# Kernel optimization log

Hardware: AMD Instinct MI355X
Metric: run time of the kernel (lower is better)

Reference implementation:

```python
import jax, jax.numpy as jnp
import numpy as np

B, S, D_IN, D_K, D_V = 4, 2048, 1024, 1024, 1024


def setup_inputs() -> dict:
    key = jax.random.key(0)
    ks = jax.random.split(key, 7)
    s_in = 1.0 / np.sqrt(D_IN)
    return {
        "x": jax.random.normal(ks[0], (B, S, D_IN), dtype=jnp.float32),
        "Wq": jax.random.uniform(ks[1], (D_K, D_IN), jnp.float32, -s_in, s_in),
        "bq": jax.random.uniform(ks[2], (D_K,), jnp.float32, -s_in, s_in),
        "Wk": jax.random.uniform(ks[3], (D_K, D_IN), jnp.float32, -s_in, s_in),
        "bk": jax.random.uniform(ks[4], (D_K,), jnp.float32, -s_in, s_in),
        "Wv": jax.random.uniform(ks[5], (D_V, D_IN), jnp.float32, -s_in, s_in),
        "bv": jax.random.uniform(ks[6], (D_V,), jnp.float32, -s_in, s_in),
    }


def reference(x, Wq, bq, Wk, bk, Wv, bv):
    # Linear: y = x @ W^T + b (torch convention, weight is [out, in])
    Q = jnp.einsum("bsd,kd->bsk", x, Wq) + bq  # [B,S,Dk]
    K = jnp.einsum("bsd,kd->bsk", x, Wk) + bk  # [B,S,Dk]
    V = jnp.einsum("bsd,vd->bsv", x, Wv) + bv  # [B,S,Dv]
    norm_fact = 1.0 / np.sqrt(D_K)
    # NOTE: faithful to original — softmax on raw scores, THEN scale by 1/sqrt(dim_k)
    scores = jnp.einsum("bqk,bsk->bqs", Q, K)          # [B,S,S]
    atten = jax.nn.softmax(scores, axis=-1) * norm_fact  # post-softmax scaling
    return jnp.einsum("bqs,bsv->bqv", atten, V)          # [B,S,Dv]
```

## Files before the change

### kernel.cpp

```cpp
#include <hip/hip_runtime.h>
#include <hip/hip_bf16.h>
#include <cstdint>
#include <cstddef>


typedef __attribute__((ext_vector_type(8))) _Float16 f16x8;
typedef __attribute__((ext_vector_type(4))) _Float16 f16x4;
typedef __attribute__((ext_vector_type(4))) float f32x4;

#define BM 128
#define BN 128
#define BK 64

#define NBATCH 4
#define SEQ 2048
#define DIM 1024
#define MTOT (NBATCH * SEQ)

__device__ __forceinline__ void async_ld16(const void* g, void* l) {
  __builtin_amdgcn_global_load_lds((__attribute__((address_space(1))) void*)(g),
                                   (__attribute__((address_space(3))) void*)(l),
                                   16, 0, 0);
}

__device__ __forceinline__ void gemm_core(const _Float16* __restrict__ A, int lda,
                                          const _Float16* __restrict__ B, int ldb,
                                          int K, int m0, int n0,
                                          _Float16* As, _Float16* Bs,
                                          f32x4 (&acc)[4][4]) {
  const int t = threadIdx.x;
  const int w = t >> 6;
  const int lrow = t & 15;
  const int quad = (t >> 4) & 3;
  const int wm = (w >> 1) << 6;
  const int wn = (w & 1) << 6;

  const int rb = t >> 3;
  const int co = (((t & 7) ^ (rb & 7)) << 3);
  const _Float16* Ap = A + (size_t)(m0 + rb) * lda + co;
  const _Float16* Bp = B + (size_t)(n0 + rb) * ldb + co;

  const int sw = lrow & 7;

  for (int k0 = 0; k0 < K; k0 += BK) {
#pragma unroll
    for (int i = 0; i < 4; ++i)
      async_ld16(Ap + (size_t)(i * 32) * lda + k0, As + i * 2048 + (w << 9));
#pragma unroll
    for (int i = 0; i < 4; ++i)
      async_ld16(Bp + (size_t)(i * 32) * ldb + k0, Bs + i * 2048 + (w << 9));
    __syncthreads();
#pragma unroll
    for (int kk = 0; kk < BK; kk += 32) {
      const int slot = ((kk >> 3) + quad) ^ sw;
      f16x8 af[4], bfr[4];
#pragma unroll
      for (int mi = 0; mi < 4; ++mi)
        af[mi] = *(const f16x8*)(As + (wm + mi * 16 + lrow) * BK + (slot << 3));
#pragma unroll
      for (int ni = 0; ni < 4; ++ni)
        bfr[ni] = *(const f16x8*)(Bs + (wn + ni * 16 + lrow) * BK + (slot << 3));
#pragma unroll
      for (int mi = 0; mi < 4; ++mi)
#pragma unroll
        for (int ni = 0; ni < 4; ++ni)
          acc[mi][ni] = __builtin_amdgcn_mfma_f32_16x16x32_f16(af[mi], bfr[ni],
                                                              acc[mi][ni], 0, 0, 0);
    }
    __syncthreads();
  }
}

__global__ __launch_bounds__(256) void split_all_kernel(
    const float* __restrict__ x, const float* __restrict__ Wq,
    const float* __restrict__ Wk, const float* __restrict__ Wv,
    _Float16* __restrict__ xh, _Float16* __restrict__ Wqh,
    _Float16* __restrict__ Wkh, _Float16* __restrict__ Wvh) {
  int r = blockIdx.x;
  const float* src;
  _Float16* dst;
  if (r < MTOT)            { src = x;  dst = xh;  }
  else if (r < MTOT + DIM) { src = Wq; dst = Wqh; r -= MTOT; }
  else if (r < MTOT + 2 * DIM) { src = Wk; dst = Wkh; r -= MTOT + DIM; }
  else                     { src = Wv; dst = Wvh; r -= MTOT + 2 * DIM; }
  const int t = threadIdx.x;
  const float4 v = ((const float4*)(src + (size_t)r * DIM))[t];
  f16x4 hi = {(_Float16)v.x, (_Float16)v.y, (_Float16)v.z, (_Float16)v.w};
  ((f16x4*)(dst + (size_t)r * DIM))[t] = hi;
}

__global__ __launch_bounds__(256, 2) void qkv_kernel(
    const _Float16* __restrict__ xh,
    const _Float16* __restrict__ Wqh, const float* __restrict__ bq,
    const _Float16* __restrict__ Wkh, const float* __restrict__ bk,
    const _Float16* __restrict__ Wvh, const float* __restrict__ bv,
    _Float16* __restrict__ Qp, _Float16* __restrict__ Kp,
    _Float16* __restrict__ Vt) {
  __shared__ alignas(16) _Float16 As[BM * BK];
  __shared__ alignas(16) _Float16 Bs[BN * BK];
  f32x4 acc[4][4] = {};
  const int l = blockIdx.x;
  const int z = l >> 9;
  const int r9 = l & 511;
  const int m0 = (((r9 & 7) | ((r9 >> 6) << 3))) * BM;
  const int n0 = ((r9 >> 3) & 7) * BN;
  const _Float16* W = (z == 0) ? Wqh : (z == 1) ? Wkh : Wvh;
  const float* bias = (z == 0) ? bq : (z == 1) ? bk : bv;
  gemm_core(xh, DIM, W, DIM, DIM, m0, n0, As, Bs, acc);

  const int t = threadIdx.x, w = t >> 6, lrow = t & 15, quad = (t >> 4) & 3;
  const int wm = (w >> 1) << 6, wn = (w & 1) << 6;
  if (z == 2) {
    const int b = m0 >> 11;
    const int s_base = (m0 & (SEQ - 1)) + wm + quad * 4;
#pragma unroll
    for (int ni = 0; ni < 4; ++ni) {
      const int col = n0 + wn + ni * 16 + lrow;
      const float bb = bias[col];
      _Float16* vrow = Vt + (size_t)((b << 10) + col) * SEQ;
#pragma unroll
      for (int mi = 0; mi < 4; ++mi) {
        f16x4 v4 = {(_Float16)(acc[mi][ni][0] + bb),
                    (_Float16)(acc[mi][ni][1] + bb),
                    (_Float16)(acc[mi][ni][2] + bb),
                    (_Float16)(acc[mi][ni][3] + bb)};
        *(f16x4*)(vrow + s_base + mi * 16) = v4;
      }
    }
  } else {
    _Float16* base = (z == 0) ? Qp : Kp;
#pragma unroll
    for (int ni = 0; ni < 4; ++ni) {
      const int col = n0 + wn + ni * 16 + lrow;
      const float bb = bias[col];
#pragma unroll
      for (int mi = 0; mi < 4; ++mi) {
#pragma unroll
        for (int r = 0; r < 4; ++r) {
          const int row = m0 + wm + mi * 16 + quad * 4 + r;
          base[(size_t)row * DIM + col] = (_Float16)(acc[mi][ni][r] + bb);
        }
      }
    }
  }
}

__global__ __launch_bounds__(256, 2) void scores_kernel(
    const _Float16* __restrict__ Qp, const _Float16* __restrict__ Kp,
    float* __restrict__ Sc) {
  __shared__ alignas(16) _Float16 As[BM * BK];
  __shared__ alignas(16) _Float16 Bs[BN * BK];
  f32x4 acc[4][4] = {};
  const int l = blockIdx.x;
  const int b = l >> 8;
  const int r8 = l & 255;
  const int s = r8 >> 6;
  const int m0 = ((r8 & 7) | ((s & 1) << 3)) * BM;
  const int n0 = (((r8 >> 3) & 7) | ((s >> 1) << 3)) * BN;
  gemm_core(Qp + (size_t)b * SEQ * DIM, DIM,
            Kp + (size_t)b * SEQ * DIM, DIM, DIM, m0, n0, As, Bs, acc);
  float* out = Sc + (size_t)b * SEQ * SEQ;
  const int t = threadIdx.x, w = t >> 6, lrow = t & 15, quad = (t >> 4) & 3;
  const int wm = (w >> 1) << 6, wn = (w & 1) << 6;
#pragma unroll
  for (int ni = 0; ni < 4; ++ni) {
    const int col = n0 + wn + ni * 16 + lrow;
#pragma unroll
    for (int mi = 0; mi < 4; ++mi) {
#pragma unroll
      for (int r = 0; r < 4; ++r) {
        const int row = m0 + wm + mi * 16 + quad * 4 + r;
        out[(size_t)row * SEQ + col] = acc[mi][ni][r];
      }
    }
  }
}

__global__ __launch_bounds__(256) void softmax_kernel(const float* __restrict__ Sc,
                                                      _Float16* __restrict__ P) {
  const int r0 = blockIdx.x * 2;
  const float* rowA = Sc + (size_t)r0 * SEQ;
  const float* rowB = rowA + SEQ;
  _Float16* prowA = P + (size_t)r0 * SEQ;
  _Float16* prowB = prowA + SEQ;
  const int t = threadIdx.x;
  const int w = t >> 6;

  const float4 a0 = ((const float4*)rowA)[t];
  const float4 a1 = ((const float4*)rowA)[t + 256];
  const float4 b0 = ((const float4*)rowB)[t];
  const float4 b1 = ((const float4*)rowB)[t + 256];

  float mA = fmaxf(fmaxf(fmaxf(a0.x, a0.y), fmaxf(a0.z, a0.w)),
                   fmaxf(fmaxf(a1.x, a1.y), fmaxf(a1.z, a1.w)));
  float mB = fmaxf(fmaxf(fmaxf(b0.x, b0.y), fmaxf(b0.z, b0.w)),
                   fmaxf(fmaxf(b1.x, b1.y), fmaxf(b1.z, b1.w)));
#pragma unroll
  for (int o = 32; o; o >>= 1) {
    mA = fmaxf(mA, __shfl_down(mA, o));
    mB = fmaxf(mB, __shfl_down(mB, o));
  }
  __shared__ float red[16];
  if ((t & 63) == 0) { red[w] = mA; red[w + 4] = mB; }
  __syncthreads();
  mA = fmaxf(fmaxf(red[0], red[1]), fmaxf(red[2], red[3]));
  mB = fmaxf(fmaxf(red[4], red[5]), fmaxf(red[6], red[7]));

  float eA[8], eB[8];
  eA[0] = __expf(a0.x - mA); eA[1] = __expf(a0.y - mA);
  eA[2] = __expf(a0.z - mA); eA[3] = __expf(a0.w - mA);
  eA[4] = __expf(a1.x - mA); eA[5] = __expf(a1.y - mA);
  eA[6] = __expf(a1.z - mA); eA[7] = __expf(a1.w - mA);
  eB[0] = __expf(b0.x - mB); eB[1] = __expf(b0.y - mB);
  eB[2] = __expf(b0.z - mB); eB[3] = __expf(b0.w - mB);
  eB[4] = __expf(b1.x - mB); eB[5] = __expf(b1.y - mB);
  eB[6] = __expf(b1.z - mB); eB[7] = __expf(b1.w - mB);
  float sA = ((eA[0] + eA[1]) + (eA[2] + eA[3])) + ((eA[4] + eA[5]) + (eA[6] + eA[7]));
  float sB = ((eB[0] + eB[1]) + (eB[2] + eB[3])) + ((eB[4] + eB[5]) + (eB[6] + eB[7]));
#pragma unroll
  for (int o = 32; o; o >>= 1) {
    sA += __shfl_down(sA, o);
    sB += __shfl_down(sB, o);
  }
  if ((t & 63) == 0) { red[8 + w] = sA; red[12 + w] = sB; }
  __syncthreads();
  sA = (red[8] + red[9]) + (red[10] + red[11]);
  sB = (red[12] + red[13]) + (red[14] + red[15]);

  const float scA = 0.03125f / sA;
  const float scB = 0.03125f / sB;
  f16x4 oA0 = {(_Float16)(eA[0] * scA), (_Float16)(eA[1] * scA),
               (_Float16)(eA[2] * scA), (_Float16)(eA[3] * scA)};
  f16x4 oA1 = {(_Float16)(eA[4] * scA), (_Float16)(eA[5] * scA),
               (_Float16)(eA[6] * scA), (_Float16)(eA[7] * scA)};
  f16x4 oB0 = {(_Float16)(eB[0] * scB), (_Float16)(eB[1] * scB),
               (_Float16)(eB[2] * scB), (_Float16)(eB[3] * scB)};
  f16x4 oB1 = {(_Float16)(eB[4] * scB), (_Float16)(eB[5] * scB),
               (_Float16)(eB[6] * scB), (_Float16)(eB[7] * scB)};
  ((f16x4*)prowA)[t] = oA0;
  ((f16x4*)prowA)[t + 256] = oA1;
  ((f16x4*)prowB)[t] = oB0;
  ((f16x4*)prowB)[t + 256] = oB1;
}

__global__ __launch_bounds__(256, 2) void pv_kernel(
    const _Float16* __restrict__ P, const _Float16* __restrict__ Vt,
    float* __restrict__ out) {
  __shared__ alignas(16) _Float16 As[BM * BK];
  __shared__ alignas(16) _Float16 Bs[BN * BK];
  f32x4 acc[4][4] = {};
  const int l = blockIdx.x;
  const int b = l >> 7;
  const int r7 = l & 127;
  const int m0 = ((r7 & 7) | ((r7 >> 6) << 3)) * BM;
  const int n0 = ((r7 >> 3) & 7) * BN;
  gemm_core(P + (size_t)b * SEQ * SEQ, SEQ,
            Vt + (size_t)b * DIM * SEQ, SEQ, SEQ, m0, n0, As, Bs, acc);
  float* ob = out + (size_t)b * SEQ * DIM;
  const int t = threadIdx.x, w = t >> 6, lrow = t & 15, quad = (t >> 4) & 3;
  const int wm = (w >> 1) << 6, wn = (w & 1) << 6;
#pragma unroll
  for (int ni = 0; ni < 4; ++ni) {
    const int col = n0 + wn + ni * 16 + lrow;
#pragma unroll
    for (int mi = 0; mi < 4; ++mi) {
#pragma unroll
      for (int r = 0; r < 4; ++r) {
        const int row = m0 + wm + mi * 16 + quad * 4 + r;
        ob[(size_t)row * DIM + col] = acc[mi][ni][r];
      }
    }
  }
}

extern "C" void kernel_launch(void* const* d_in, const int* in_sizes, int n_in,
                              void* d_out, int out_size, void* d_ws, size_t ws_size,
                              hipStream_t stream) {
  const float* x  = (const float*)d_in[0];
  const float* Wq = (const float*)d_in[1];
  const float* bq = (const float*)d_in[2];
  const float* Wk = (const float*)d_in[3];
  const float* bk = (const float*)d_in[4];
  const float* Wv = (const float*)d_in[5];
  const float* bv = (const float*)d_in[6];
  float* out = (float*)d_out;

  char* ws = (char*)d_ws;
  _Float16* Qp  = (_Float16*)(ws);
  _Float16* Kp  = (_Float16*)(ws + 16777216);
  _Float16* Vt  = (_Float16*)(ws + 33554432);
  float*    Sc  = (float*)(ws + 50331648);
  _Float16* P   = (_Float16*)(ws + 117440512);
  _Float16* xh  = (_Float16*)(ws + 50331648);
  _Float16* Wqh = (_Float16*)(ws + 67108864);
  _Float16* Wkh = (_Float16*)(ws + 69206016);
  _Float16* Wvh = (_Float16*)(ws + 71303168);

  dim3 blk(256, 1, 1);
  split_all_kernel<<<dim3(MTOT + 3 * DIM), blk, 0, stream>>>(
      x, Wq, Wk, Wv, xh, Wqh, Wkh, Wvh);
  qkv_kernel<<<dim3(3 * 512), blk, 0, stream>>>(
      xh, Wqh, bq, Wkh, bk, Wvh, bv, Qp, Kp, Vt);
  scores_kernel<<<dim3(NBATCH * 256), blk, 0, stream>>>(Qp, Kp, Sc);
  softmax_kernel<<<dim3(MTOT / 2), blk, 0, stream>>>(Sc, P);
  pv_kernel<<<dim3(NBATCH * 128), blk, 0, stream>>>(P, Vt, out);
}
```

Baseline: 247.3 us.

## Use 128x256 tiles with 8 waves and triple-buffered async LDS pipeline

Replaces the single-buffered GEMM core with a triple-buffered pipeline that prefetches two K-tiles ahead, using explicit vmcnt waits and raw barriers so global loads overlap MFMA work. Tiles grow to 128x256 with 512-thread blocks and one block per CU, and QKV treats the three weight matrices as one concatenated matrix, which relies on Wq, Wk and Wv sitting contiguously in the workspace. Block-to-tile mappings are remapped around XCD interleaving for cache locality. The larger tiles use 144KB of LDS per block and give fewer blocks (256 in the PV GEMM), which risks lower occupancy and tail imbalance.

```diff
diff --git a/kernel.cpp b/kernel.cpp
--- a/kernel.cpp
+++ b/kernel.cpp
@@ -9,8 +9,10 @@
 typedef __attribute__((ext_vector_type(4))) float f32x4;
 
 #define BM 128
-#define BN 128
+#define BN 256
 #define BK 64
+#define A_TILE (BM * BK)
+#define B_TILE (BN * BK)
 
 #define NBATCH 4
 #define SEQ 2048
@@ -23,51 +25,82 @@
                                    16, 0, 0);
 }
 
-__device__ __forceinline__ void gemm_core(const _Float16* __restrict__ A, int lda,
-                                          const _Float16* __restrict__ B, int ldb,
-                                          int K, int m0, int n0,
-                                          _Float16* As, _Float16* Bs,
-                                          f32x4 (&acc)[4][4]) {
+__device__ __forceinline__ void stage_tile(const _Float16* __restrict__ Ap, int lda,
+                                           const _Float16* __restrict__ Bp, int ldb,
+                                           int k0, _Float16* As, _Float16* Bs,
+                                           int w) {
+#pragma unroll
+  for (int i = 0; i < 2; ++i)
+    async_ld16(Ap + (size_t)(i * 64) * lda + k0, As + i * 4096 + (w << 9));
+#pragma unroll
+  for (int i = 0; i < 4; ++i)
+    async_ld16(Bp + (size_t)(i * 64) * ldb + k0, Bs + i * 4096 + (w << 9));
+}
+
+__device__ __forceinline__ void gemm8(const _Float16* __restrict__ A, int lda,
+                                      const _Float16* __restrict__ B, int ldb,
+                                      int K, int m0, int n0,
+                                      _Float16* sA, _Float16* sB,
+                                      f32x4 (&acc)[4][4]) {
   const int t = threadIdx.x;
   const int w = t >> 6;
   const int lrow = t & 15;
   const int quad = (t >> 4) & 3;
-  const int wm = (w >> 1) << 6;
-  const int wn = (w & 1) << 6;
-
+  const int wm = (w >> 2) << 6;
+  const int wn = (w & 3) << 6;
   const int rb = t >> 3;
   const int co = (((t & 7) ^ (rb & 7)) << 3);
   const _Float16* Ap = A + (size_t)(m0 + rb) * lda + co;
   const _Float16* Bp = B + (size_t)(n0 + rb) * ldb + co;
-
   const int sw = lrow & 7;
 
-  for (int k0 = 0; k0 < K; k0 += BK) {
-#pragma unroll
-    for (int i = 0; i < 4; ++i)
-      async_ld16(Ap + (size_t)(i * 32) * lda + k0, As + i * 2048 + (w << 9));
-#pragma unroll
-    for (int i = 0; i < 4; ++i)
-      async_ld16(Bp + (size_t)(i * 32) * ldb + k0, Bs + i * 2048 + (w << 9));
-    __syncthreads();
+  _Float16 *A0 = sA, *A1 = sA + A_TILE, *A2 = sA + 2 * A_TILE;
+  _Float16 *B0 = sB, *B1 = sB + B_TILE, *B2 = sB + 2 * B_TILE;
+
+  const int nt = K >> 6;
+  stage_tile(Ap, lda, Bp, ldb, 0, A0, B0, w);
+  stage_tile(Ap, lda, Bp, ldb, BK, A1, B1, w);
+
+  for (int tt = 0; tt < nt; ++tt) {
+    if (tt + 2 < nt) {
+      stage_tile(Ap, lda, Bp, ldb, (tt + 2) * BK, A2, B2, w);
+      asm volatile("s_waitcnt vmcnt(12)" ::: "memory");
+    } else if (tt + 1 < nt) {
+      asm volatile("s_waitcnt vmcnt(6)" ::: "memory");
+    } else {
+      asm volatile("s_waitcnt vmcnt(0)" ::: "memory");
+    }
+    asm volatile("" ::: "memory");
+    __builtin_amdgcn_s_barrier();
+    asm volatile("" ::: "memory");
+    __builtin_amdgcn_sched_barrier(0);
+
 #pragma unroll
     for (int kk = 0; kk < BK; kk += 32) {
       const int slot = ((kk >> 3) + quad) ^ sw;
-      f16x8 af[4], bfr[4];
+      f16x8 af[4], bf[4];
 #pragma unroll
       for (int mi = 0; mi < 4; ++mi)
-        af[mi] = *(const f16x8*)(As + (wm + mi * 16 + lrow) * BK + (slot << 3));
+        af[mi] = *(const f16x8*)(A0 + (wm + mi * 16 + lrow) * BK + (slot << 3));
 #pragma unroll
       for (int ni = 0; ni < 4; ++ni)
-        bfr[ni] = *(const f16x8*)(Bs + (wn + ni * 16 + lrow) * BK + (slot << 3));
+        bf[ni] = *(const f16x8*)(B0 + (wn + ni * 16 + lrow) * BK + (slot << 3));
+      __builtin_amdgcn_s_setprio(1);
 #pragma unroll
       for (int mi = 0; mi < 4; ++mi)
 #pragma unroll
         for (int ni = 0; ni < 4; ++ni)
-          acc[mi][ni] = __builtin_amdgcn_mfma_f32_16x16x32_f16(af[mi], bfr[ni],
-                                                              acc[mi][ni], 0, 0, 0);
-    }
-    __syncthreads();
+          acc[mi][ni] = __builtin_amdgcn_mfma_f32_16x16x32_f16(af[mi], bf[ni],
+                                                               acc[mi][ni], 0, 0, 0);
+      __builtin_amdgcn_s_setprio(0);
+    }
+
+    asm volatile("" ::: "memory");
+    __builtin_amdgcn_s_barrier();
+    asm volatile("" ::: "memory");
+    __builtin_amdgcn_sched_barrier(0);
+    _Float16* ta = A0; A0 = A1; A1 = A2; A2 = ta;
+    _Float16* tb = B0; B0 = B1; B1 = B2; B2 = tb;
   }
 }
 
@@ -89,34 +122,33 @@
   ((f16x4*)(dst + (size_t)r * DIM))[t] = hi;
 }
 
-__global__ __launch_bounds__(256, 2) void qkv_kernel(
-    const _Float16* __restrict__ xh,
-    const _Float16* __restrict__ Wqh, const float* __restrict__ bq,
-    const _Float16* __restrict__ Wkh, const float* __restrict__ bk,
-    const _Float16* __restrict__ Wvh, const float* __restrict__ bv,
+__global__ __launch_bounds__(512, 1) void qkv_kernel(
+    const _Float16* __restrict__ xh, const _Float16* __restrict__ Wcat,
+    const float* __restrict__ bq, const float* __restrict__ bk,
+    const float* __restrict__ bv,
     _Float16* __restrict__ Qp, _Float16* __restrict__ Kp,
     _Float16* __restrict__ Vt) {
-  __shared__ alignas(16) _Float16 As[BM * BK];
-  __shared__ alignas(16) _Float16 Bs[BN * BK];
+  __shared__ alignas(16) _Float16 sA[3 * A_TILE];
+  __shared__ alignas(16) _Float16 sB[3 * B_TILE];
   f32x4 acc[4][4] = {};
   const int l = blockIdx.x;
-  const int z = l >> 9;
-  const int r9 = l & 511;
-  const int m0 = (((r9 & 7) | ((r9 >> 6) << 3))) * BM;
-  const int n0 = ((r9 >> 3) & 7) * BN;
-  const _Float16* W = (z == 0) ? Wqh : (z == 1) ? Wkh : Wvh;
-  const float* bias = (z == 0) ? bq : (z == 1) ? bk : bv;
-  gemm_core(xh, DIM, W, DIM, DIM, m0, n0, As, Bs, acc);
+  const int xcd = l & 7;
+  const int i = l >> 3;
+  const int m0 = (xcd * 8 + (i & 7)) * BM;
+  const int n0 = (i >> 3) * BN;
+  gemm8(xh, DIM, Wcat, DIM, DIM, m0, n0, sA, sB, acc);
 
   const int t = threadIdx.x, w = t >> 6, lrow = t & 15, quad = (t >> 4) & 3;
-  const int wm = (w >> 1) << 6, wn = (w & 1) << 6;
+  const int wm = (w >> 2) << 6, wn = (w & 3) << 6;
+  const int z = n0 >> 10;
+  const int ncol = (n0 & 1023) + wn;
   if (z == 2) {
     const int b = m0 >> 11;
     const int s_base = (m0 & (SEQ - 1)) + wm + quad * 4;
 #pragma unroll
     for (int ni = 0; ni < 4; ++ni) {
-      const int col = n0 + wn + ni * 16 + lrow;
-      const float bb = bias[col];
+      const int col = ncol + ni * 16 + lrow;
+      const float bb = bv[col];
       _Float16* vrow = Vt + (size_t)((b << 10) + col) * SEQ;
 #pragma unroll
       for (int mi = 0; mi < 4; ++mi) {
@@ -128,10 +160,11 @@
       }
     }
   } else {
+    const float* bias = (z == 0) ? bq : bk;
     _Float16* base = (z == 0) ? Qp : Kp;
 #pragma unroll
     for (int ni = 0; ni < 4; ++ni) {
-      const int col = n0 + wn + ni * 16 + lrow;
+      const int col = ncol + ni * 16 + lrow;
       const float bb = bias[col];
 #pragma unroll
       for (int mi = 0; mi < 4; ++mi) {
@@ -145,32 +178,33 @@
   }
 }
 
-__global__ __launch_bounds__(256, 2) void scores_kernel(
+__global__ __launch_bounds__(512, 1) void scores_kernel(
     const _Float16* __restrict__ Qp, const _Float16* __restrict__ Kp,
     float* __restrict__ Sc) {
-  __shared__ alignas(16) _Float16 As[BM * BK];
-  __shared__ alignas(16) _Float16 Bs[BN * BK];
+  __shared__ alignas(16) _Float16 sA[3 * A_TILE];
+  __shared__ alignas(16) _Float16 sB[3 * B_TILE];
   f32x4 acc[4][4] = {};
   const int l = blockIdx.x;
-  const int b = l >> 8;
-  const int r8 = l & 255;
-  const int s = r8 >> 6;
-  const int m0 = ((r8 & 7) | ((s & 1) << 3)) * BM;
-  const int n0 = (((r8 >> 3) & 7) | ((s >> 1) << 3)) * BN;
-  gemm_core(Qp + (size_t)b * SEQ * DIM, DIM,
-            Kp + (size_t)b * SEQ * DIM, DIM, DIM, m0, n0, As, Bs, acc);
+  const int b = l >> 7;
+  const int r = l & 127;
+  const int xcd = r & 7;
+  const int i = r >> 3;
+  const int m0 = ((xcd & 1) * 8 + (i & 7)) * BM;
+  const int n0 = (((xcd >> 1) << 1) + (i >> 3)) * BN;
+  gemm8(Qp + (size_t)b * SEQ * DIM, DIM,
+        Kp + (size_t)b * SEQ * DIM, DIM, DIM, m0, n0, sA, sB, acc);
   float* out = Sc + (size_t)b * SEQ * SEQ;
   const int t = threadIdx.x, w = t >> 6, lrow = t & 15, quad = (t >> 4) & 3;
-  const int wm = (w >> 1) << 6, wn = (w & 1) << 6;
+  const int wm = (w >> 2) << 6, wn = (w & 3) << 6;
 #pragma unroll
   for (int ni = 0; ni < 4; ++ni) {
     const int col = n0 + wn + ni * 16 + lrow;
 #pragma unroll
     for (int mi = 0; mi < 4; ++mi) {
 #pragma unroll
-      for (int r = 0; r < 4; ++r) {
-        const int row = m0 + wm + mi * 16 + quad * 4 + r;
-        out[(size_t)row * SEQ + col] = acc[mi][ni][r];
+      for (int r2 = 0; r2 < 4; ++r2) {
+        const int row = m0 + wm + mi * 16 + quad * 4 + r2;
+        out[(size_t)row * SEQ + col] = acc[mi][ni][r2];
       }
     }
   }
@@ -243,31 +277,33 @@
   ((f16x4*)prowB)[t + 256] = oB1;
 }
 
-__global__ __launch_bounds__(256, 2) void pv_kernel(
+__global__ __launch_bounds__(512, 1) void pv_kernel(
     const _Float16* __restrict__ P, const _Float16* __restrict__ Vt,
     float* __restrict__ out) {
-  __shared__ alignas(16) _Float16 As[BM * BK];
-  __shared__ alignas(16) _Float16 Bs[BN * BK];
+  __shared__ alignas(16) _Float16 sA[3 * A_TILE];
+  __shared__ alignas(16) _Float16 sB[3 * B_TILE];
   f32x4 acc[4][4] = {};
   const int l = blockIdx.x;
-  const int b = l >> 7;
-  const int r7 = l & 127;
-  const int m0 = ((r7 & 7) | ((r7 >> 6) << 3)) * BM;
-  const int n0 = ((r7 >> 3) & 7) * BN;
-  gemm_core(P + (size_t)b * SEQ * SEQ, SEQ,
-            Vt + (size_t)b * DIM * SEQ, SEQ, SEQ, m0, n0, As, Bs, acc);
+  const int b = l >> 6;
+  const int r = l & 63;
+  const int xcd = r & 7;
+  const int i = r >> 3;
+  const int m0 = ((xcd & 3) * 4 + (i & 3)) * BM;
+  const int n0 = (((xcd >> 2) << 1) + (i >> 2)) * BN;
+  gemm8(P + (size_t)b * SEQ * SEQ, SEQ,
+        Vt + (size_t)b * DIM * SEQ, SEQ, SEQ, m0, n0, sA, sB, acc);
   float* ob = out + (size_t)b * SEQ * DIM;
   const int t = threadIdx.x, w = t >> 6, lrow = t & 15, quad = (t >> 4) & 3;
-  const int wm = (w >> 1) << 6, wn = (w & 1) << 6;
+  const int wm = (w >> 2) << 6, wn = (w & 3) << 6;
 #pragma unroll
   for (int ni = 0; ni < 4; ++ni) {
     const int col = n0 + wn + ni * 16 + lrow;
 #pragma unroll
     for (int mi = 0; mi < 4; ++mi) {
 #pragma unroll
-      for (int r = 0; r < 4; ++r) {
-        const int row = m0 + wm + mi * 16 + quad * 4 + r;
-        ob[(size_t)row * DIM + col] = acc[mi][ni][r];
+      for (int r2 = 0; r2 < 4; ++r2) {
+        const int row = m0 + wm + mi * 16 + quad * 4 + r2;
+        ob[(size_t)row * DIM + col] = acc[mi][ni][r2];
       }
     }
   }
@@ -296,12 +332,11 @@
   _Float16* Wkh = (_Float16*)(ws + 69206016);
   _Float16* Wvh = (_Float16*)(ws + 71303168);
 
-  dim3 blk(256, 1, 1);
-  split_all_kernel<<<dim3(MTOT + 3 * DIM), blk, 0, stream>>>(
+  split_all_kernel<<<dim3(MTOT + 3 * DIM), dim3(256), 0, stream>>>(
       x, Wq, Wk, Wv, xh, Wqh, Wkh, Wvh);
-  qkv_kernel<<<dim3(3 * 512), blk, 0, stream>>>(
-      xh, Wqh, bq, Wkh, bk, Wvh, bv, Qp, Kp, Vt);
-  scores_kernel<<<dim3(NBATCH * 256), blk, 0, stream>>>(Qp, Kp, Sc);
-  softmax_kernel<<<dim3(MTOT / 2), blk, 0, stream>>>(Sc, P);
-  pv_kernel<<<dim3(NBATCH * 128), blk, 0, stream>>>(P, Vt, out);
-}
+  qkv_kernel<<<dim3(768), dim3(512), 0, stream>>>(
+      xh, Wqh, bq, bk, bv, Qp, Kp, Vt);
+  scores_kernel<<<dim3(512), dim3(512), 0, stream>>>(Qp, Kp, Sc);
+  softmax_kernel<<<dim3(MTOT / 2), dim3(256), 0, stream>>>(Sc, P);
+  pv_kernel<<<dim3(256), dim3(512), 0, stream>>>(P, Vt, out);
+}
```

After: 288.9 us. 1.17x slower.
